# Kernel tuning notes

Hardware: AMD Instinct MI355X
Metric: run time of the kernel (lower is better)

Reference implementation:

```python
import jax, jax.numpy as jnp
import numpy as np

DIM = 1024
CTX_DIM = 1024
HEADS = 16
DIM_HEAD = 64
INNER = HEADS * DIM_HEAD  # 1024
FF_INNER = 4 * DIM        # 4096
EPS = 1e-5


def layer_norm(x, g, b):
    mu = jnp.mean(x, axis=-1, keepdims=True)
    var = jnp.var(x, axis=-1, keepdims=True)
    return (x - mu) * jax.lax.rsqrt(var + EPS) * g + b


def setup_inputs() -> dict:
    key = jax.random.key(0)
    ks = jax.random.split(key, 9)
    b, n, j = 4, 2048, 1024
    inp = {
        "x": jax.random.normal(ks[0], (b, n, DIM), dtype=jnp.float32),
        "context": jax.random.normal(ks[1], (b, j, CTX_DIM), dtype=jnp.float32),
        "ln_g": jnp.ones((DIM,), jnp.float32),
        "ln_b": jnp.zeros((DIM,), jnp.float32),
        "cln_g": jnp.ones((CTX_DIM,), jnp.float32),
        "cln_b": jnp.zeros((CTX_DIM,), jnp.float32),
        "Wq": jax.random.normal(ks[2], (DIM, INNER), dtype=jnp.float32) * (DIM ** -0.5),
        "Wkv": jax.random.normal(ks[3], (CTX_DIM, 2 * DIM_HEAD), dtype=jnp.float32) * (CTX_DIM ** -0.5),
        "Wo": jax.random.normal(ks[4], (INNER, DIM), dtype=jnp.float32) * (INNER ** -0.5),
        "Wff1": jax.random.normal(ks[5], (DIM, 2 * FF_INNER), dtype=jnp.float32) * (DIM ** -0.5),
        "Wff2": jax.random.normal(ks[6], (FF_INNER, DIM), dtype=jnp.float32) * (FF_INNER ** -0.5),
    }
    return inp


def reference(x, context, ln_g, ln_b, cln_g, cln_b, Wq, Wkv, Wo, Wff1, Wff2):
    scale = DIM_HEAD ** -0.5
    xn = layer_norm(x, ln_g, ln_b)                       # [b, n, dim]
    cn = layer_norm(context, cln_g, cln_b)               # [b, j, ctx_dim]
    b, n, _ = xn.shape
    q = (xn @ Wq).reshape(b, n, HEADS, DIM_HEAD).transpose(0, 2, 1, 3) * scale  # [b,h,n,d]
    kv = cn @ Wkv                                        # [b, j, 2d]
    k, v = kv[..., :DIM_HEAD], kv[..., DIM_HEAD:]        # [b, j, d] each (shared head)
    sim = jnp.einsum('bhid,bjd->bhij', q, k)
    attn = jax.nn.softmax(sim, axis=-1)
    out = jnp.einsum('bhij,bjd->bhid', attn, v)          # [b,h,n,d]
    out = out.transpose(0, 2, 1, 3).reshape(b, n, INNER) @ Wo  # [b,n,dim]
    # parallel SwiGLU FF on normed x
    ff = xn @ Wff1                                       # [b,n,2*ff_inner]
    h, gate = ff[..., :FF_INNER], ff[..., FF_INNER:]
    out = out + (jax.nn.silu(gate) * h) @ Wff2
    return out
```

## Files before the change

### kernel.cpp

```cpp
#include <hip/hip_runtime.h>
#include <math.h>

typedef unsigned short u16;
typedef __attribute__((ext_vector_type(8))) short short8;
typedef __attribute__((ext_vector_type(8))) unsigned short ushortx8;
typedef __attribute__((ext_vector_type(4))) unsigned short ushortx4;
typedef __attribute__((ext_vector_type(4))) float floatx4;

#define DEVI __device__ __forceinline__

DEVI float bf2f(u16 u) {
    unsigned int i = ((unsigned int)u) << 16;
    float f; __builtin_memcpy(&f, &i, 4); return f;
}
DEVI u16 f2bf(float f) {
    unsigned int i; __builtin_memcpy(&i, &f, 4);
    i += 0x7fffu + ((i >> 16) & 1u);
    return (u16)(i >> 16);
}
DEVI void gl_lds16(const void* g, void* l) {
    __builtin_amdgcn_global_load_lds(
        (const __attribute__((address_space(1))) void*)g,
        (__attribute__((address_space(3))) void*)l, 16, 0, 0);
}

template <bool FF1>
__global__ void transpose_kernel(const float* __restrict__ B, u16* __restrict__ BT,
                                 int K, int N) {
    __shared__ u16 t[32][33];
    int nb = blockIdx.x * 32, kb = blockIdx.y * 32;
    int tx = threadIdx.x, ty = threadIdx.y;
    for (int i = ty; i < 32; i += 8)
        t[i][tx] = f2bf(B[(size_t)(kb + i) * N + nb + tx]);
    __syncthreads();
    for (int i = ty; i < 32; i += 8) {
        int c = nb + i;
        int r_out = FF1 ? ((((c & 4095) >> 4) << 5) + ((c >> 12) << 4) + (c & 15)) : c;
        BT[(size_t)r_out * K + kb + tx] = t[tx][i];
    }
}

__global__ __launch_bounds__(256)
void ln_kernel(const float* __restrict__ x, const float* __restrict__ g,
               const float* __restrict__ b, u16* __restrict__ out) {
    __shared__ float sw[4], sw2[4];
    const int tid = threadIdx.x, wave = tid >> 6, lane = tid & 63;
    const float* xr = x + (size_t)blockIdx.x * 1024;
    float4 v = *(const float4*)(xr + tid * 4);
    float f[4] = {v.x, v.y, v.z, v.w};
    float s = f[0] + f[1] + f[2] + f[3];
    float s2 = f[0]*f[0] + f[1]*f[1] + f[2]*f[2] + f[3]*f[3];
    for (int o = 32; o; o >>= 1) {
        s  += __shfl_xor(s,  o, 64);
        s2 += __shfl_xor(s2, o, 64);
    }
    if (lane == 0) { sw[wave] = s; sw2[wave] = s2; }
    __syncthreads();
    float tot  = sw[0] + sw[1] + sw[2] + sw[3];
    float tot2 = sw2[0] + sw2[1] + sw2[2] + sw2[3];
    float mu  = tot * (1.f / 1024.f);
    float var = tot2 * (1.f / 1024.f) - mu * mu;
    float rs  = rsqrtf(var + 1e-5f);
    float4 gv = *(const float4*)(g + tid * 4);
    float4 bv = *(const float4*)(b + tid * 4);
    ushortx4 ov;
    ov[0] = f2bf((f[0] - mu) * rs * gv.x + bv.x);
    ov[1] = f2bf((f[1] - mu) * rs * gv.y + bv.y);
    ov[2] = f2bf((f[2] - mu) * rs * gv.z + bv.z);
    ov[3] = f2bf((f[3] - mu) * rs * gv.w + bv.w);
    *(ushortx4*)(out + (size_t)blockIdx.x * 1024 + tid * 4) = ov;
}

enum { EPI_PLAIN = 0, EPI_Q = 1, EPI_KV = 2, EPI_ADD_F32 = 3 };

template <int EPI>
__global__ __launch_bounds__(256)
void gemm_bt_kernel(const u16* __restrict__ A, const u16* __restrict__ BT,
                    void* __restrict__ Cv, u16* __restrict__ AUX,
                    int M, int N, int K) {
    __shared__ u16 As[128 * 32];
    __shared__ u16 Bs[128 * 32];
    const int tid = threadIdx.x, wave = tid >> 6, lane = tid & 63;
    const int mbase = blockIdx.x * 128, nbase = blockIdx.y * 128;
    const int m0 = (wave & 1) * 64, n0 = (wave >> 1) * 64;
    const int lrow = lane & 15, lq = lane >> 4;

    floatx4 zero = {0.f, 0.f, 0.f, 0.f};
    floatx4 acc[4][4];
#pragma unroll
    for (int i = 0; i < 4; i++)
#pragma unroll
        for (int j = 0; j < 4; j++) acc[i][j] = zero;

    for (int kt = 0; kt < K; kt += 32) {
#pragma unroll
        for (int i = 0; i < 2; i++) {
            int e = i * 2048 + tid * 8;
            int r = e >> 5, c = e & 31;
            gl_lds16(A  + (size_t)(mbase + r) * K + kt + c, As + e);
            gl_lds16(BT + (size_t)(nbase + r) * K + kt + c, Bs + e);
        }
        __syncthreads();
        short8 af[4], bf[4];
#pragma unroll
        for (int f = 0; f < 4; f++) {
            af[f] = *(const short8*)(As + (m0 + f * 16 + lrow) * 32 + lq * 8);
            bf[f] = *(const short8*)(Bs + (n0 + f * 16 + lrow) * 32 + lq * 8);
        }
#pragma unroll
        for (int i = 0; i < 4; i++)
#pragma unroll
            for (int j = 0; j < 4; j++)
                acc[i][j] = __builtin_amdgcn_mfma_f32_16x16x32_bf16(af[i], bf[j], acc[i][j], 0, 0, 0);
        __syncthreads();
    }

#pragma unroll
    for (int mf = 0; mf < 4; mf++)
#pragma unroll
        for (int nf = 0; nf < 4; nf++)
#pragma unroll
            for (int r = 0; r < 4; r++) {
                int row = mbase + m0 + mf * 16 + lq * 4 + r;
                int col = nbase + n0 + nf * 16 + lrow;
                float v = acc[mf][nf][r];
                if constexpr (EPI == EPI_PLAIN) {
                    ((u16*)Cv)[(size_t)row * N + col] = f2bf(v);
                } else if constexpr (EPI == EPI_Q) {
                    int b = row >> 11, i2 = row & 2047, h = col >> 6, d = col & 63;
                    ((u16*)Cv)[((size_t)((b * 16 + h) * 2048 + i2)) * 64 + d] = f2bf(v * 0.125f);
                } else if constexpr (EPI == EPI_KV) {
                    int b = row >> 10, j = row & 1023;
                    if (col < 64) ((u16*)Cv)[(size_t)row * 64 + col] = f2bf(v);
                    else AUX[((size_t)(b * 64 + (col - 64))) * 1024 + j] = f2bf(v);
                } else {
                    ((float*)Cv)[(size_t)row * N + col] = v + bf2f(AUX[(size_t)row * N + col]);
                }
            }
}

__global__ __launch_bounds__(512, 2)
void gemm256_ff1_kernel(const u16* __restrict__ A, const u16* __restrict__ BT,
                        u16* __restrict__ C, int K) {
    extern __shared__ float4 smem4[];
    char* smem = (char*)smem4;

    const int tid = threadIdx.x, wave = tid >> 6, lane = tid & 63;
    const int wm = wave >> 2, wn = wave & 3;
    const int lrow = lane & 15, lq = lane >> 4;

    const int bid = blockIdx.x;
    const int wg = (bid & 7) * 128 + (bid >> 3);
    const int mbase = (wg & 31) * 256, nbase = (wg >> 5) * 256;

    const int srow  = tid >> 2;
    const int sslot = (tid & 3) ^ ((tid >> 3) & 3);
    const u16* aS = A  + (size_t)(mbase + srow) * K + sslot * 8;
    const u16* bS = BT + (size_t)(nbase + srow) * K + sslot * 8;
    const size_t chunkK = (size_t)128 * K;
    char* dst0 = smem + tid * 16;

#define STAGE(t_, kt_) do {                                   \
        char* db_ = dst0 + ((t_) & 3) * 32768;                \
        gl_lds16(aS + (kt_),          db_);                   \
        gl_lds16(aS + chunkK + (kt_), db_ + 8192);            \
        gl_lds16(bS + (kt_),          db_ + 16384);           \
        gl_lds16(bS + chunkK + (kt_), db_ + 24576);           \
    } while (0)

    floatx4 zero = {0.f, 0.f, 0.f, 0.f};
    floatx4 acc[8][4];
#pragma unroll
    for (int i = 0; i < 8; i++)
#pragma unroll
        for (int j = 0; j < 4; j++) acc[i][j] = zero;

    const int NT = K >> 5;
    STAGE(0, 0);
    STAGE(1, 32);

    const int swb = (lq ^ ((lrow >> 1) & 3)) * 16;
    const int aRow = wm * 128 + lrow;
    const int bRow = wn * 64 + lrow;

    for (int t = 0; t < NT; ++t) {
        if (t + 1 < NT) { asm volatile("s_waitcnt vmcnt(4)" ::: "memory"); }
        else            { asm volatile("s_waitcnt vmcnt(0)" ::: "memory"); }
        asm volatile("s_waitcnt lgkmcnt(0)" ::: "memory");
        __builtin_amdgcn_s_barrier();
        asm volatile("" ::: "memory");

        if (t + 2 < NT) STAGE(t + 2, (t + 2) * 32);

        const char* buf = smem + (t & 3) * 32768;
        const char* Ab = buf + (size_t)aRow * 64 + swb;
        const char* Bb = buf + 16384 + (size_t)bRow * 64 + swb;
        short8 af[8], bf[4];
#pragma unroll
        for (int mf = 0; mf < 8; ++mf) af[mf] = *(const short8*)(Ab + mf * 1024);
#pragma unroll
        for (int nf = 0; nf < 4; ++nf) bf[nf] = *(const short8*)(Bb + nf * 1024);

        __builtin_amdgcn_s_setprio(1);
#pragma unroll
        for (int mf = 0; mf < 8; ++mf)
#pragma unroll
            for (int nf = 0; nf < 4; ++nf)
                acc[mf][nf] = __builtin_amdgcn_mfma_f32_16x16x32_bf16(af[mf], bf[nf], acc[mf][nf], 0, 0, 0);
        __builtin_amdgcn_s_setprio(0);
    }
#undef STAGE

    const int orow0 = mbase + wm * 128;
    const int pcol0 = (nbase + wn * 64) >> 1;
#pragma unroll
    for (int mf = 0; mf < 8; ++mf)
#pragma unroll
        for (int p = 0; p < 2; ++p)
#pragma unroll
            for (int r = 0; r < 4; ++r) {
                float hv = acc[mf][2 * p][r], gv = acc[mf][2 * p + 1][r];
                float act = hv * (gv / (1.f + __expf(-gv)));
                int row = orow0 + mf * 16 + lq * 4 + r;
                int col = pcol0 + p * 16 + lrow;
                C[(size_t)row * 4096 + col] = f2bf(act);
            }
}

__global__ __launch_bounds__(256)
void attn_kernel(const u16* __restrict__ q, const u16* __restrict__ k,
                 const u16* __restrict__ vt, u16* __restrict__ o) {
    __shared__ char smem[53248];
    u16* Qs  = (u16*)smem;
    u16* Ps  = (u16*)smem;
    u16* Ks  = (u16*)(smem + 17408);
    u16* VTs = (u16*)(smem + 35840);
    float* Lp   = (float*)(smem + 17408);
    float* Ltot = (float*)(smem + 18432);

    const int tid = threadIdx.x, wave = tid >> 6, lane = tid & 63;
    const int lrow = lane & 15, lq = lane >> 4;
    const int b = blockIdx.z, h = blockIdx.y, mt = blockIdx.x;

    const u16* qb = q + ((size_t)((b * 16 + h) * 2048) + mt * 64) * 64;
    const u16* kb = k + (size_t)b * 1024 * 64;
    const u16* vb = vt + (size_t)b * 64 * 1024;

#pragma unroll
    for (int i = 0; i < 2; i++) {
        int e = i * 2048 + tid * 8;
        int r = e >> 6, d = e & 63;
        *(ushortx8*)(Qs + r * 72 + d) = *(const ushortx8*)(qb + e);
    }
    __syncthreads();
    short8 qf[2][4];
#pragma unroll
    for (int ks = 0; ks < 2; ks++)
#pragma unroll
        for (int cf = 0; cf < 4; cf++)
            qf[ks][cf] = *(const short8*)(Qs + (cf * 16 + lrow) * 72 + ks * 32 + lq * 8);

    floatx4 zero = {0.f, 0.f, 0.f, 0.f};
    floatx4 oacc[4];
#pragma unroll
    for (int i = 0; i < 4; i++) oacc[i] = zero;
    float lsum[4] = {0.f, 0.f, 0.f, 0.f};

    for (int jt = 0; jt < 8; jt++) {
#pragma unroll
        for (int i = 0; i < 4; i++) {
            int e = i * 2048 + tid * 8;
            int r = e >> 6, d = e & 63;
            *(ushortx8*)(Ks + r * 72 + d) = *(const ushortx8*)(kb + jt * 8192 + e);
            int dv = e >> 7, jj = e & 127;
            *(ushortx8*)(VTs + dv * 136 + jj) =
                *(const ushortx8*)(vb + (size_t)dv * 1024 + jt * 128 + jj);
        }
        __syncthreads();

        floatx4 sacc[2][4];
#pragma unroll
        for (int rf = 0; rf < 2; rf++)
#pragma unroll
            for (int cf = 0; cf < 4; cf++) sacc[rf][cf] = zero;
#pragma unroll
        for (int ks = 0; ks < 2; ks++) {
            short8 af[2];
#pragma unroll
            for (int rf = 0; rf < 2; rf++)
                af[rf] = *(const short8*)(Ks + (wave * 32 + rf * 16 + lrow) * 72 + ks * 32 + lq * 8);
#pragma unroll
            for (int rf = 0; rf < 2; rf++)
#pragma unroll
                for (int cf = 0; cf < 4; cf++)
                    sacc[rf][cf] = __builtin_amdgcn_mfma_f32_16x16x32_bf16(af[rf], qf[ks][cf], sacc[rf][cf], 0, 0, 0);
        }

#pragma unroll
        for (int rf = 0; rf < 2; rf++)
#pragma unroll
            for (int cf = 0; cf < 4; cf++) {
                float p0 = __expf(sacc[rf][cf][0]);
                float p1 = __expf(sacc[rf][cf][1]);
                float p2 = __expf(sacc[rf][cf][2]);
                float p3 = __expf(sacc[rf][cf][3]);
                lsum[cf] += p0 + p1 + p2 + p3;
                ushortx4 pk = {f2bf(p0), f2bf(p1), f2bf(p2), f2bf(p3)};
                int m = cf * 16 + lrow;
                int j0 = wave * 32 + rf * 16 + lq * 4;
                *(ushortx4*)(Ps + m * 136 + j0) = pk;
            }
        __syncthreads();

#pragma unroll
        for (int ks = 0; ks < 4; ks++) {
            short8 pf[4];
#pragma unroll
            for (int mf = 0; mf < 4; mf++)
                pf[mf] = *(const short8*)(Ps + (mf * 16 + lrow) * 136 + ks * 32 + lq * 8);
            short8 vf = *(const short8*)(VTs + (wave * 16 + lrow) * 136 + ks * 32 + lq * 8);
#pragma unroll
            for (int mf = 0; mf < 4; mf++)
                oacc[mf] = __builtin_amdgcn_mfma_f32_16x16x32_bf16(pf[mf], vf, oacc[mf], 0, 0, 0);
        }
        __syncthreads();
    }

    float lv[4];
#pragma unroll
    for (int cf = 0; cf < 4; cf++) {
        float v = lsum[cf];
        v += __shfl_xor(v, 16, 64);
        v += __shfl_xor(v, 32, 64);
        lv[cf] = v;
    }
    if (lane < 16) {
#pragma unroll
        for (int cf = 0; cf < 4; cf++) Lp[wave * 64 + cf * 16 + lane] = lv[cf];
    }
    __syncthreads();
    if (tid < 64) Ltot[tid] = Lp[tid] + Lp[64 + tid] + Lp[128 + tid] + Lp[192 + tid];
    __syncthreads();

    const int d = wave * 16 + lrow;
    const size_t orow0 = (size_t)(b * 2048 + mt * 64);
#pragma unroll
    for (int mf = 0; mf < 4; mf++)
#pragma unroll
        for (int r = 0; r < 4; r++) {
            int m = mf * 16 + lq * 4 + r;
            float val = oacc[mf][r] / Ltot[m];
            o[(orow0 + m) * 1024 + h * 64 + d] = f2bf(val);
        }
}

extern "C" void kernel_launch(void* const* d_in, const int* in_sizes, int n_in,
                              void* d_out, int out_size, void* d_ws, size_t ws_size,
                              hipStream_t stream) {
    const float* x     = (const float*)d_in[0];
    const float* ctx   = (const float*)d_in[1];
    const float* ln_g  = (const float*)d_in[2];
    const float* ln_b  = (const float*)d_in[3];
    const float* cln_g = (const float*)d_in[4];
    const float* cln_b = (const float*)d_in[5];
    const float* Wq    = (const float*)d_in[6];
    const float* Wkv   = (const float*)d_in[7];
    const float* Wo    = (const float*)d_in[8];
    const float* Wff1  = (const float*)d_in[9];
    const float* Wff2  = (const float*)d_in[10];
    (void)in_sizes; (void)n_in; (void)out_size; (void)ws_size;

    u16* ws = (u16*)d_ws;
    const size_t MiB = 524288;
    u16* ffa   = ws;
    u16* qb    = ws;
    u16* attnb = ws + 16 * MiB;
    u16* cn    = ws + 32 * MiB;
    u16* kb    = ws + 40 * MiB;
    u16* vtb   = ws + 40 * MiB + 262144;
    u16* WqT   = ws + 41 * MiB;
    u16* WkvT  = ws + 43 * MiB;
    u16* WoT   = ws + 44 * MiB;
    u16* xn    = ws + 64 * MiB;
    u16* wo    = ws + 80 * MiB;
    u16* Wff1T = ws + 96 * MiB;
    u16* Wff2T = ws + 112 * MiB;

    static bool attr_set = false;
    if (!attr_set) {
        hipFuncSetAttribute(reinterpret_cast<const void*>(gemm256_ff1_kernel),
                            hipFuncAttributeMaxDynamicSharedMemorySize, 131072);
        attr_set = true;
    }

    dim3 tb(32, 8);
    transpose_kernel<false><<<dim3(32, 32),  tb, 0, stream>>>(Wq,   WqT,   1024, 1024);
    transpose_kernel<false><<<dim3(4, 32),   tb, 0, stream>>>(Wkv,  WkvT,  1024, 128);
    transpose_kernel<false><<<dim3(32, 32),  tb, 0, stream>>>(Wo,   WoT,   1024, 1024);
    transpose_kernel<true> <<<dim3(256, 32), tb, 0, stream>>>(Wff1, Wff1T, 1024, 8192);
    transpose_kernel<false><<<dim3(32, 128), tb, 0, stream>>>(Wff2, Wff2T, 4096, 1024);

    ln_kernel<<<8192, 256, 0, stream>>>(x,   ln_g,  ln_b,  xn);
    ln_kernel<<<4096, 256, 0, stream>>>(ctx, cln_g, cln_b, cn);

    gemm_bt_kernel<EPI_Q> <<<dim3(64, 8), 256, 0, stream>>>(xn, WqT,  qb, nullptr, 8192, 1024, 1024);
    gemm_bt_kernel<EPI_KV><<<dim3(32, 1), 256, 0, stream>>>(cn, WkvT, kb, vtb,     4096, 128,  1024);

    attn_kernel<<<dim3(32, 16, 4), 256, 0, stream>>>(qb, kb, vtb, attnb);

    gemm_bt_kernel<EPI_PLAIN><<<dim3(64, 8), 256, 0, stream>>>(attnb, WoT, wo, nullptr, 8192, 1024, 1024);
    gemm256_ff1_kernel<<<dim3(1024), 512, 131072, stream>>>(xn, Wff1T, ffa, 1024);
    gemm_bt_kernel<EPI_ADD_F32><<<dim3(64, 8), 256, 0, stream>>>(ffa, Wff2T, d_out, wo, 8192, 1024, 4096);
}
```

Measured before the change: 590.2 us.

## Restructure FF1 GEMM into quadrant-staged 8-wave ping-pong pipeline with BK=64

```diff
diff --git a/kernel.cpp b/kernel.cpp
--- a/kernel.cpp
+++ b/kernel.cpp
@@ -153,78 +153,115 @@
     const int wg = (bid & 7) * 128 + (bid >> 3);
     const int mbase = (wg & 31) * 256, nbase = (wg >> 5) * 256;
 
-    const int srow  = tid >> 2;
-    const int sslot = (tid & 3) ^ ((tid >> 3) & 3);
-    const u16* aS = A  + (size_t)(mbase + srow) * K + sslot * 8;
-    const u16* bS = BT + (size_t)(nbase + srow) * K + sslot * 8;
-    const size_t chunkK = (size_t)128 * K;
+    const int sl = (tid & 7) ^ ((tid >> 3) & 7);
+    const u16* aBase = A  + (size_t)(mbase + (tid >> 3)) * K + sl * 8;
+    const u16* bBase = BT + (size_t)(nbase + (tid >> 3)) * K + sl * 8;
     char* dst0 = smem + tid * 16;
 
-#define STAGE(t_, kt_) do {                                   \
-        char* db_ = dst0 + ((t_) & 3) * 32768;                \
-        gl_lds16(aS + (kt_),          db_);                   \
-        gl_lds16(aS + chunkK + (kt_), db_ + 8192);            \
-        gl_lds16(bS + (kt_),          db_ + 16384);           \
-        gl_lds16(bS + chunkK + (kt_), db_ + 24576);           \
+#define STAGE_A(buf_, h_, kt_) do {                                        \
+        char* d_ = dst0 + (buf_) * 65536 + (h_) * 16384;                   \
+        gl_lds16(aBase + (size_t)(h_) * 128 * K + (kt_), d_);              \
+        gl_lds16(aBase + (size_t)((h_) * 128 + 64) * K + (kt_), d_ + 8192);\
     } while (0)
+#define STAGE_B(buf_, h_, kt_) do {                                        \
+        char* d_ = dst0 + 32768 + (buf_) * 65536 + (h_) * 16384;           \
+        gl_lds16(bBase + (size_t)(h_) * 128 * K + (kt_), d_);              \
+        gl_lds16(bBase + (size_t)((h_) * 128 + 64) * K + (kt_), d_ + 8192);\
+    } while (0)
+#define BAR() do { asm volatile("" ::: "memory");                          \
+        __builtin_amdgcn_s_barrier();                                      \
+        asm volatile("" ::: "memory"); } while (0)
+#define LGKM0() do { asm volatile("s_waitcnt lgkmcnt(0)" ::: "memory");    \
+        __builtin_amdgcn_sched_barrier(0); } while (0)
+#define MFMA16(Q, BF) do {                                                 \
+        __builtin_amdgcn_s_setprio(1);                                     \
+        _Pragma("unroll") for (int mf_ = 0; mf_ < 4; ++mf_)                \
+        _Pragma("unroll") for (int nf_ = 0; nf_ < 2; ++nf_)                \
+        _Pragma("unroll") for (int ks_ = 0; ks_ < 2; ++ks_)                \
+            acc[Q][mf_][nf_] = __builtin_amdgcn_mfma_f32_16x16x32_bf16(    \
+                af[mf_][ks_], BF[nf_][ks_], acc[Q][mf_][nf_], 0, 0, 0);    \
+        __builtin_amdgcn_s_setprio(0); } while (0)
+#define READ_A(H) do { _Pragma("unroll") for (int mf_ = 0; mf_ < 4; ++mf_){\
+        af[mf_][0] = *(const short8*)(Ab + (H) * 16384 + mf_ * 2048 + cb0);\
+        af[mf_][1] = *(const short8*)(Ab + (H) * 16384 + mf_ * 2048 + cb1);\
+    } } while (0)
+#define READ_B(DST, H) do { _Pragma("unroll") for (int nf_ = 0; nf_ < 2; ++nf_){\
+        DST[nf_][0] = *(const short8*)(Bb + (H) * 16384 + nf_ * 2048 + cb0);\
+        DST[nf_][1] = *(const short8*)(Bb + (H) * 16384 + nf_ * 2048 + cb1);\
+    } } while (0)
 
     floatx4 zero = {0.f, 0.f, 0.f, 0.f};
-    floatx4 acc[8][4];
-#pragma unroll
-    for (int i = 0; i < 8; i++)
-#pragma unroll
-        for (int j = 0; j < 4; j++) acc[i][j] = zero;
-
-    const int NT = K >> 5;
-    STAGE(0, 0);
-    STAGE(1, 32);
-
-    const int swb = (lq ^ ((lrow >> 1) & 3)) * 16;
-    const int aRow = wm * 128 + lrow;
-    const int bRow = wn * 64 + lrow;
+    floatx4 acc[4][4][2];
+#pragma unroll
+    for (int q = 0; q < 4; ++q)
+#pragma unroll
+        for (int i = 0; i < 4; ++i)
+#pragma unroll
+            for (int j = 0; j < 2; ++j) acc[q][i][j] = zero;
+
+    const int cb0 = ((0 + lq) ^ (lrow & 7)) << 4;
+    const int cb1 = ((4 + lq) ^ (lrow & 7)) << 4;
+
+    const int NT = K >> 6;
+
+    STAGE_A(0, 0, 0); STAGE_B(0, 0, 0); STAGE_A(0, 1, 0); STAGE_B(0, 1, 0);
+    STAGE_A(1, 0, 64); STAGE_B(1, 0, 64);
+    asm volatile("s_waitcnt vmcnt(4)" ::: "memory");
+    BAR();
 
     for (int t = 0; t < NT; ++t) {
-        if (t + 1 < NT) { asm volatile("s_waitcnt vmcnt(4)" ::: "memory"); }
-        else            { asm volatile("s_waitcnt vmcnt(0)" ::: "memory"); }
-        asm volatile("s_waitcnt lgkmcnt(0)" ::: "memory");
-        __builtin_amdgcn_s_barrier();
-        asm volatile("" ::: "memory");
-
-        if (t + 2 < NT) STAGE(t + 2, (t + 2) * 32);
-
-        const char* buf = smem + (t & 3) * 32768;
-        const char* Ab = buf + (size_t)aRow * 64 + swb;
-        const char* Bb = buf + 16384 + (size_t)bRow * 64 + swb;
-        short8 af[8], bf[4];
-#pragma unroll
-        for (int mf = 0; mf < 8; ++mf) af[mf] = *(const short8*)(Ab + mf * 1024);
-#pragma unroll
-        for (int nf = 0; nf < 4; ++nf) bf[nf] = *(const short8*)(Bb + nf * 1024);
-
-        __builtin_amdgcn_s_setprio(1);
-#pragma unroll
-        for (int mf = 0; mf < 8; ++mf)
-#pragma unroll
-            for (int nf = 0; nf < 4; ++nf)
-                acc[mf][nf] = __builtin_amdgcn_mfma_f32_16x16x32_bf16(af[mf], bf[nf], acc[mf][nf], 0, 0, 0);
-        __builtin_amdgcn_s_setprio(0);
-    }
-#undef STAGE
-
-    const int orow0 = mbase + wm * 128;
-    const int pcol0 = (nbase + wn * 64) >> 1;
-#pragma unroll
-    for (int mf = 0; mf < 8; ++mf)
-#pragma unroll
-        for (int p = 0; p < 2; ++p)
+        const int bu = t & 1;
+        const char* Ab = smem + bu * 65536 + (size_t)((wm * 64 + lrow) * 128);
+        const char* Bb = smem + bu * 65536 + 32768 + (size_t)((wn * 32 + lrow) * 128);
+        short8 af[4][2], bf0[2][2], bf1[2][2];
+
+        READ_A(0); READ_B(bf0, 0);
+        if (t + 1 < NT) STAGE_A(bu ^ 1, 1, (t + 1) * 64);
+        BAR(); LGKM0();
+        MFMA16(0, bf0);
+        BAR();
+
+        READ_B(bf1, 1);
+        if (t + 1 < NT) STAGE_B(bu ^ 1, 1, (t + 1) * 64);
+        BAR(); LGKM0();
+        MFMA16(1, bf1);
+        BAR();
+
+        READ_A(1);
+        if (t + 2 < NT) STAGE_A(bu, 0, (t + 2) * 64);
+        BAR(); LGKM0();
+        MFMA16(2, bf0);
+        BAR();
+
+        if (t + 2 < NT) STAGE_B(bu, 0, (t + 2) * 64);
+        MFMA16(3, bf1);
+        asm volatile("s_waitcnt vmcnt(4)" ::: "memory");
+        BAR();
+    }
+#undef STAGE_A
+#undef STAGE_B
+#undef BAR
+#undef LGKM0
+#undef MFMA16
+#undef READ_A
+#undef READ_B
+
+    const int orow = mbase + wm * 64 + lq * 4;
+    const int og16 = (nbase >> 5) + wn;
+#pragma unroll
+    for (int q = 0; q < 4; ++q) {
+        const int qm = q >> 1, qn = q & 1;
+#pragma unroll
+        for (int mf = 0; mf < 4; ++mf)
 #pragma unroll
             for (int r = 0; r < 4; ++r) {
-                float hv = acc[mf][2 * p][r], gv = acc[mf][2 * p + 1][r];
+                float hv = acc[q][mf][0][r], gv = acc[q][mf][1][r];
                 float act = hv * (gv / (1.f + __expf(-gv)));
-                int row = orow0 + mf * 16 + lq * 4 + r;
-                int col = pcol0 + p * 16 + lrow;
+                int row = orow + qm * 128 + mf * 16 + r;
+                int col = (og16 + qn * 4) * 16 + lrow;
                 C[(size_t)row * 4096 + col] = f2bf(act);
             }
+    }
 }
 
 __global__ __launch_bounds__(256)
```

After: 598.9 us. Within noise of the previous version (+1.5%).
